# Performance work log

Measured on AMD Instinct MI355X. Metric: run time of the kernel, lower is better.

Reference implementation:

```python
import jax, jax.numpy as jnp
import numpy as np

# --- ConductanceLIFConfig defaults (normalized units, threshold = 1.0) ---
DT_MS = 1.0
C_M = 1.0
G_L = 0.05
E_L = 0.0
E_E = 3.0
E_I = -0.5
E_ADAPT = -0.5
V_RESET = 0.0
TAU_E = 5.0
TAU_I = 10.0
TAU_ADAPT = 100.0
ADAPT_INC = 0.0
NOISE_STD = 0.02
NOISE_TAU = 5.0

GE_DECAY = float(np.exp(-DT_MS / TAU_E))
GI_DECAY = float(np.exp(-DT_MS / TAU_I))
GA_DECAY = float(np.exp(-DT_MS / TAU_ADAPT))
OU_ALPHA = float(np.exp(-DT_MS / NOISE_TAU))
OU_SIGMA = float(NOISE_STD * np.sqrt(1.0 - OU_ALPHA ** 2))  # stationary-variance OU drive

T = 512
N = 65536


def setup_inputs() -> dict:
    key = jax.random.key(0)
    k1, k2, k3, k4 = jax.random.split(key, 4)
    # synaptic conductance inputs per step, normalized by g_L (sparse-ish, small positive)
    g_exc = 0.2 * jax.random.uniform(k1, (T, N), dtype=jnp.float32)
    g_inh = 0.1 * jax.random.uniform(k2, (T, N), dtype=jnp.float32)
    noise = jax.random.normal(k3, (T, N), dtype=jnp.float32)  # white driver for OU process
    v_threshold = jnp.ones((N,), dtype=jnp.float32)
    # tau_ref ~ Normal(5, 2) clamped to [3.0, 8.0], as in __init__
    tau_ref = jnp.clip(5.0 + 2.0 * jax.random.normal(k4, (N,), dtype=jnp.float32), 3.0, 8.0)
    return {"g_exc": g_exc, "g_inh": g_inh, "noise": noise,
            "v_threshold": v_threshold, "tau_ref": tau_ref}


def reference(g_exc, g_inh, noise, v_threshold, tau_ref):
    """T-step conductance-based LIF scan. Returns (spikes [T,N] bool, membranes [T,N] f32)."""

    def step(carry, inp):
        v, gE, gI, gA, ref, ou = carry
        ge_in, gi_in, z = inp
        # exponential conductance decay + input accumulation (units of g_L)
        gE = gE * GE_DECAY + ge_in
        gI = gI * GI_DECAY + gi_in
        gA = gA * GA_DECAY
        # exponential-Euler membrane update toward V_inf
        g_tot_rel = 1.0 + gE + gI + gA                      # total conductance / g_L
        v_inf = (E_L + gE * E_E + gI * E_I + gA * E_ADAPT) / g_tot_rel
        decay = jnp.exp(-(DT_MS * G_L / C_M) * g_tot_rel)
        v = v_inf + (v - v_inf) * decay
        # OU membrane noise
        ou = ou * OU_ALPHA + OU_SIGMA * z
        v = v + ou
        # refractory clamp
        in_ref = ref > 0.0
        v = jnp.where(in_ref, V_RESET, v)
        # spike, reset, refractory restart, adaptation increment
        spike = (v >= v_threshold) & (~in_ref)
        v = jnp.where(spike, V_RESET, v)
        ref = jnp.where(spike, tau_ref, jnp.maximum(ref - DT_MS, 0.0))
        gA = gA + ADAPT_INC * spike.astype(v.dtype)
        return (v, gE, gI, gA, ref, ou), (spike, v)

    z = jnp.zeros((N,), dtype=jnp.float32)
    carry0 = (z, z, z, z, z, z)  # v, g_E, g_I, g_adapt, refractory, ou
    _, (spikes, membranes) = jax.lax.scan(step, carry0, (g_exc, g_inh, noise))
    return spikes, membranes
```

## Files before the change

### kernel.cpp

```cpp
#include <hip/hip_runtime.h>
#include <cmath>


__device__ __forceinline__ void gload_lds(const float* g, float* l) {
    __builtin_amdgcn_global_load_lds(
        (const __attribute__((address_space(1))) unsigned int*)(const void*)g,
        (__attribute__((address_space(3))) unsigned int*)(void*)l,
        4, 0, 0);
}

#define WAITV(n) asm volatile("s_waitcnt vmcnt(" #n ")" ::: "memory")

__global__ __launch_bounds__(256, 1) void lif_scan(
    const float* __restrict__ g_exc,
    const float* __restrict__ g_inh,
    const float* __restrict__ noise,
    const float* __restrict__ v_th,
    const float* __restrict__ tau_ref,
    float* __restrict__ out_spk,
    float* __restrict__ out_mem,
    int N, int T,
    float cGE, float cGI, float cALPHA, float cSIGMA)
{
    __shared__ float smem[16][3][256];

    const int tid = threadIdx.x;
    const int wq  = (tid >> 6) << 6;
    const int n   = blockIdx.x * 256 + tid;

    const float vth = v_th[n];
    const float trf = tau_ref[n];

    float v = 0.f, gE = 0.f, gI = 0.f, ref = 0.f, ou = 0.f;

    auto issueB = [&](int t0, int sb) {
        #pragma unroll
        for (int k = 0; k < 4; ++k) {
            const size_t row = (size_t)(t0 + k) * (size_t)N + (size_t)n;
            gload_lds(g_exc + row, &smem[sb + k][0][wq]);
            gload_lds(g_inh + row, &smem[sb + k][1][wq]);
            gload_lds(noise + row, &smem[sb + k][2][wq]);
        }
    };

    auto step = [&](float ge_in, float gi_in, float z, int tt) {
        gE = __builtin_fmaf(gE, cGE, ge_in);
        gI = __builtin_fmaf(gI, cGI, gi_in);

        const float gt  = 1.0f + gE + gI;
        const float num = __builtin_fmaf(gI, -0.5f, gE * 3.0f);
        const float vinf = num * __builtin_amdgcn_rcpf(gt);

        const float decay = __expf(-0.05f * gt);

        v = __builtin_fmaf(v - vinf, decay, vinf);

        ou = __builtin_fmaf(ou, cALPHA, cSIGMA * z);
        v = v + ou;

        const bool in_ref = (ref > 0.0f);
        const bool spike  = (v >= vth) && (!in_ref);
        v = (in_ref || spike) ? 0.0f : v;
        ref = spike ? trf : fmaxf(ref - 1.0f, 0.0f);

        const size_t off = (size_t)tt * (size_t)N + (size_t)n;
        __builtin_nontemporal_store(spike ? 1.0f : 0.0f, out_spk + off);
        __builtin_nontemporal_store(v, out_mem + off);
    };

    auto group = [&](int t0, int sb, bool issue) {
        float vals[12];
        #pragma unroll
        for (int k = 0; k < 4; ++k) {
            vals[k * 3 + 0] = smem[sb + k][0][tid];
            vals[k * 3 + 1] = smem[sb + k][1][tid];
            vals[k * 3 + 2] = smem[sb + k][2][tid];
        }
        asm volatile("s_waitcnt lgkmcnt(0)" ::: "memory");
        if (issue) issueB(t0 + 16, sb);
        #pragma unroll
        for (int k = 0; k < 4; ++k)
            step(vals[k * 3 + 0], vals[k * 3 + 1], vals[k * 3 + 2], t0 + k);
    };

    issueB(0, 0);
    issueB(4, 4);
    issueB(8, 8);
    issueB(12, 12);

    for (int p = 0; p <= 30; ++p) {
        WAITV(36); group(16 * p,      0,  true);
        WAITV(36); group(16 * p + 4,  4,  true);
        WAITV(36); group(16 * p + 8,  8,  true);
        WAITV(36); group(16 * p + 12, 12, true);
    }
    WAITV(36); group(496, 0,  false);
    WAITV(24); group(500, 4,  false);
    WAITV(12); group(504, 8,  false);
    WAITV(0);  group(508, 12, false);
}

extern "C" void kernel_launch(void* const* d_in, const int* in_sizes, int n_in,
                              void* d_out, int out_size, void* d_ws, size_t ws_size,
                              hipStream_t stream) {
    const float* g_exc   = (const float*)d_in[0];
    const float* g_inh   = (const float*)d_in[1];
    const float* noise   = (const float*)d_in[2];
    const float* v_th    = (const float*)d_in[3];
    const float* tau_ref = (const float*)d_in[4];

    const int N = in_sizes[3];
    const int T = in_sizes[0] / N;

    float* out_spk = (float*)d_out;
    float* out_mem = (float*)d_out + (size_t)T * (size_t)N;

    const double ge_decay = exp(-1.0 / 5.0);
    const double gi_decay = exp(-1.0 / 10.0);
    const double ou_alpha = exp(-1.0 / 5.0);
    const double ou_sigma = 0.02 * sqrt(1.0 - ou_alpha * ou_alpha);

    const int block = 256;
    const int grid = (N + block - 1) / block;
    lif_scan<<<grid, block, 0, stream>>>(
        g_exc, g_inh, noise, v_th, tau_ref, out_spk, out_mem,
        N, T,
        (float)ge_decay, (float)gi_decay, (float)ou_alpha, (float)ou_sigma);
}
```

Baseline: 126.3 us.

## Split wave halves across input streams and outputs to halve memory instructions

Each wavefront now covers 32 neurons instead of 64. The low half of the wave loads g_exc and writes membranes, and the high half loads g_inh and writes spikes. Noise rows are fetched two time steps per load instruction, one per half. This cuts global load and store instructions per wave, and the grid doubles with launch bounds allowing two blocks per CU for more concurrency. In exchange the per-neuron arithmetic is done twice within each wave, and the kernel already streams close to HBM bandwidth, which limits what it can gain.

```diff
diff --git a/kernel.cpp b/kernel.cpp
--- a/kernel.cpp
+++ b/kernel.cpp
@@ -2,7 +2,7 @@
 #include <cmath>
 
 
-__device__ __forceinline__ void gload_lds(const float* g, float* l) {
+__device__ __forceinline__ void gload_lds4(const float* g, float* l) {
     __builtin_amdgcn_global_load_lds(
         (const __attribute__((address_space(1))) unsigned int*)(const void*)g,
         (__attribute__((address_space(3))) unsigned int*)(void*)l,
@@ -11,7 +11,7 @@
 
 #define WAITV(n) asm volatile("s_waitcnt vmcnt(" #n ")" ::: "memory")
 
-__global__ __launch_bounds__(256, 1) void lif_scan(
+__global__ __launch_bounds__(256, 2) void lif_scan(
     const float* __restrict__ g_exc,
     const float* __restrict__ g_inh,
     const float* __restrict__ noise,
@@ -22,25 +22,34 @@
     int N, int T,
     float cGE, float cGI, float cALPHA, float cSIGMA)
 {
-    __shared__ float smem[16][3][256];
+    __shared__ float gegi[16][4][64];
+    __shared__ float zs[8][4][64];
 
-    const int tid = threadIdx.x;
-    const int wq  = (tid >> 6) << 6;
-    const int n   = blockIdx.x * 256 + tid;
+    const int tid  = threadIdx.x;
+    const int lane = tid & 63;
+    const int wid  = tid >> 6;
+    const int li   = lane & 31;
+    const bool hi  = (lane & 32) != 0;
 
-    const float vth = v_th[n];
-    const float trf = tau_ref[n];
+    const int W  = blockIdx.x * 4 + wid;
+    const int nb = W * 32 + li;
+
+    const float* __restrict__ baseAB = (hi ? g_inh : g_exc) + nb;
+    const float* __restrict__ baseZ  = noise + nb + (hi ? N : 0);
+    float* __restrict__ baseOut      = (hi ? out_spk : out_mem) + nb;
+
+    const float vth = v_th[nb];
+    const float trf = tau_ref[nb];
 
     float v = 0.f, gE = 0.f, gI = 0.f, ref = 0.f, ou = 0.f;
 
-    auto issueB = [&](int t0, int sb) {
+    auto issueB = [&](int tb, int sb) {
         #pragma unroll
-        for (int k = 0; k < 4; ++k) {
-            const size_t row = (size_t)(t0 + k) * (size_t)N + (size_t)n;
-            gload_lds(g_exc + row, &smem[sb + k][0][wq]);
-            gload_lds(g_inh + row, &smem[sb + k][1][wq]);
-            gload_lds(noise + row, &smem[sb + k][2][wq]);
-        }
+        for (int k = 0; k < 4; ++k)
+            gload_lds4(baseAB + (size_t)(tb + k) * (size_t)N, &gegi[sb + k][wid][0]);
+        #pragma unroll
+        for (int j = 0; j < 2; ++j)
+            gload_lds4(baseZ + (size_t)(tb + 2 * j) * (size_t)N, &zs[(sb >> 1) + j][wid][0]);
     };
 
     auto step = [&](float ge_in, float gi_in, float z, int tt) {
@@ -63,24 +72,24 @@
         v = (in_ref || spike) ? 0.0f : v;
         ref = spike ? trf : fmaxf(ref - 1.0f, 0.0f);
 
-        const size_t off = (size_t)tt * (size_t)N + (size_t)n;
-        __builtin_nontemporal_store(spike ? 1.0f : 0.0f, out_spk + off);
-        __builtin_nontemporal_store(v, out_mem + off);
+        const float outval = hi ? (spike ? 1.0f : 0.0f) : v;
+        __builtin_nontemporal_store(outval, baseOut + (size_t)tt * (size_t)N);
     };
 
     auto group = [&](int t0, int sb, bool issue) {
-        float vals[12];
+        float ge4[4], gi4[4], z4[4];
         #pragma unroll
         for (int k = 0; k < 4; ++k) {
-            vals[k * 3 + 0] = smem[sb + k][0][tid];
-            vals[k * 3 + 1] = smem[sb + k][1][tid];
-            vals[k * 3 + 2] = smem[sb + k][2][tid];
+            const int s = sb + k;
+            ge4[k] = gegi[s][wid][li];
+            gi4[k] = gegi[s][wid][32 + li];
+            z4[k]  = zs[s >> 1][wid][((s & 1) << 5) + li];
         }
         asm volatile("s_waitcnt lgkmcnt(0)" ::: "memory");
         if (issue) issueB(t0 + 16, sb);
         #pragma unroll
         for (int k = 0; k < 4; ++k)
-            step(vals[k * 3 + 0], vals[k * 3 + 1], vals[k * 3 + 2], t0 + k);
+            step(ge4[k], gi4[k], z4[k], t0 + k);
     };
 
     issueB(0, 0);
@@ -89,14 +98,14 @@
     issueB(12, 12);
 
     for (int p = 0; p <= 30; ++p) {
-        WAITV(36); group(16 * p,      0,  true);
-        WAITV(36); group(16 * p + 4,  4,  true);
-        WAITV(36); group(16 * p + 8,  8,  true);
-        WAITV(36); group(16 * p + 12, 12, true);
+        WAITV(18); group(16 * p,      0,  true);
+        WAITV(18); group(16 * p + 4,  4,  true);
+        WAITV(18); group(16 * p + 8,  8,  true);
+        WAITV(18); group(16 * p + 12, 12, true);
     }
-    WAITV(36); group(496, 0,  false);
-    WAITV(24); group(500, 4,  false);
-    WAITV(12); group(504, 8,  false);
+    WAITV(18); group(496, 0,  false);
+    WAITV(12); group(500, 4,  false);
+    WAITV(6);  group(504, 8,  false);
     WAITV(0);  group(508, 12, false);
 }
 
@@ -121,7 +130,7 @@
     const double ou_sigma = 0.02 * sqrt(1.0 - ou_alpha * ou_alpha);
 
     const int block = 256;
-    const int grid = (N + block - 1) / block;
+    const int grid  = N / 128;
     lif_scan<<<grid, block, 0, stream>>>(
         g_exc, g_inh, noise, v_th, tau_ref, out_spk, out_mem,
         N, T,
```

Measured after the change: 128.7 us. No clear change (+1.9%).
